# Kernel optimization log

Measured on AMD Instinct MI355X. Metric: run time of the kernel, lower is better.

The kernel has to match this reference:

```python
import jax, jax.numpy as jnp
import numpy as np

N = 100000
E = 1600000
F_IN = 128
HID = 32
HEADS = 4
NCLS = 64
NEG_SLOPE = 0.2
EPS = 1e-16


def setup_inputs() -> dict:
    key = jax.random.key(0)
    ks = jax.random.split(key, 12)
    inp = jax.random.normal(ks[0], (N, F_IN), dtype=jnp.float32)
    edge_index = jax.random.randint(ks[1], (2, E), 0, N, dtype=jnp.int64)
    s1 = 1.0 / np.sqrt(F_IN)
    W1 = jax.random.uniform(ks[2], (F_IN, HEADS, HID), jnp.float32, -s1, s1)
    att_src1 = jax.random.normal(ks[3], (HEADS, HID), dtype=jnp.float32) * s1
    att_dst1 = jax.random.normal(ks[4], (HEADS, HID), dtype=jnp.float32) * s1
    bias1 = jnp.zeros((HEADS * HID,), dtype=jnp.float32)
    d2 = HEADS * HID
    s2 = 1.0 / np.sqrt(d2)
    W2 = jax.random.uniform(ks[5], (d2, 1, NCLS), jnp.float32, -s2, s2)
    att_src2 = jax.random.normal(ks[6], (1, NCLS), dtype=jnp.float32) * s2
    att_dst2 = jax.random.normal(ks[7], (1, NCLS), dtype=jnp.float32) * s2
    bias2 = jnp.zeros((NCLS,), dtype=jnp.float32)
    return {"inp": inp, "edge_index": edge_index, "W1": W1, "att_src1": att_src1,
            "att_dst1": att_dst1, "bias1": bias1, "W2": W2, "att_src2": att_src2,
            "att_dst2": att_dst2, "bias2": bias2}


def _gat_layer(x, src, dst, W, a_src, a_dst, bias):
    # x: [N, F]; W: [F, H, C]
    h = jnp.einsum('nf,fhc->nhc', x, W)            # [N, H, C]
    a_s = jnp.sum(h * a_src[None], axis=-1)        # [N, H]
    a_d = jnp.sum(h * a_dst[None], axis=-1)        # [N, H]
    e = a_s[src] + a_d[dst]                        # [Etot, H]
    e = jnp.where(e >= 0, e, NEG_SLOPE * e)        # LeakyReLU(0.2)
    # softmax normalized per destination node (segment softmax)
    m = jax.ops.segment_max(e, dst, num_segments=N)      # [N, H]
    ex = jnp.exp(e - m[dst])
    denom = jax.ops.segment_sum(ex, dst, num_segments=N)  # [N, H]
    alpha = ex / (denom[dst] + EPS)                # [Etot, H]
    msg = h[src] * alpha[..., None]                # [Etot, H, C]
    out = jax.ops.segment_sum(msg, dst, num_segments=N)   # [N, H, C]
    return out.reshape(N, -1) + bias


def reference(inp, edge_index, W1, att_src1, att_dst1, bias1, W2, att_src2, att_dst2, bias2):
    # add self-loops (PyG GATConv default)
    loop = jnp.arange(N, dtype=edge_index.dtype)
    src = jnp.concatenate([edge_index[0], loop])
    dst = jnp.concatenate([edge_index[1], loop])
    x = _gat_layer(inp, src, dst, W1, att_src1, att_dst1, bias1)   # [N, H*HID]
    x = _gat_layer(x, src, dst, W2, att_src2, att_dst2, bias2)     # [N, NCLS]
    return x
```

## Files before the change

kernel.cpp:

```cpp
#include <hip/hip_runtime.h>

#define N_NODES 100000
#define F1 128
#define NCLS 64
#define EPB 8

typedef __attribute__((ext_vector_type(8))) short bf16x8;
typedef __attribute__((ext_vector_type(4))) float f32x4;

__device__ __forceinline__ unsigned f2bf(float x) {
    unsigned u = __builtin_bit_cast(unsigned, x);
    u += 0x7fff + ((u >> 16) & 1);
    return u >> 16;
}
__device__ __forceinline__ float bflo(unsigned u) {
    return __builtin_bit_cast(float, u << 16);
}
__device__ __forceinline__ float bfhi(unsigned u) {
    return __builtin_bit_cast(float, u & 0xffff0000u);
}

#define SWZ_I(v, off) __builtin_amdgcn_ds_swizzle((v), (off))
#define SWZ_F(v, off) __builtin_bit_cast(float, __builtin_amdgcn_ds_swizzle(__builtin_bit_cast(int, (v)), (off)))

__device__ __forceinline__ int load_edge(const int* ei, int is64, long long idx) {
    return is64 ? ei[2 * idx] : ei[idx];
}

#define EDGE_PROBE(ei, s_is64, tid) { \
    int v_ = (ei)[2 * ((tid) & 63) + 1]; \
    unsigned long long b_ = __ballot(v_ == 0); \
    if ((tid) == 0) s_is64 = (b_ == ~0ull) ? 1 : 0; }

__global__ __launch_bounds__(256) void histA_kernel(
        const int* __restrict__ ei, int* __restrict__ ghBM, int EB, int E) {
    __shared__ int bins[256];
    __shared__ int s_is64;
    int tid = threadIdx.x;
    bins[tid] = 0;
    EDGE_PROBE(ei, s_is64, tid)
    __syncthreads();
    int is64 = s_is64;
    long long base = (long long)blockIdx.x * 2048 + tid * EPB;
    int d[EPB];
    #pragma unroll
    for (int k = 0; k < EPB; ++k) {
        long long e = base + k;
        d[k] = (e < E) ? load_edge(ei, is64, (long long)E + e) : -1;
    }
    #pragma unroll
    for (int k = 0; k < EPB; ++k)
        if (d[k] >= 0) atomicAdd(&bins[d[k] >> 9], 1);
    __syncthreads();
    ghBM[(size_t)tid * EB + blockIdx.x] = bins[tid];
}

#define SCAN_BLOCK 1024
__global__ void pscanA_kernel(int* __restrict__ g, int* __restrict__ bsum, int K) {
    __shared__ int sm[SCAN_BLOCK];
    int tid = threadIdx.x;
    int i = blockIdx.x * SCAN_BLOCK + tid;
    int v = (i < K) ? g[i] : 0;
    sm[tid] = v;
    __syncthreads();
    for (int off = 1; off < SCAN_BLOCK; off <<= 1) {
        int t = (tid >= off) ? sm[tid - off] : 0;
        __syncthreads();
        sm[tid] += t;
        __syncthreads();
    }
    if (i < K) g[i] = sm[tid] - v;
    if (tid == SCAN_BLOCK - 1) bsum[blockIdx.x] = sm[tid];
}

__global__ void pscanC_kernel(int* __restrict__ g, const int* __restrict__ bsum,
                              int K, int nb) {
    __shared__ int sm[256];
    int tid = threadIdx.x;
    if (tid < 256) sm[tid] = (tid < nb) ? bsum[tid] : 0;
    __syncthreads();
    for (int off = 1; off < 256; off <<= 1) {
        int t = (tid < 256 && tid >= off) ? sm[tid - off] : 0;
        __syncthreads();
        if (tid < 256) sm[tid] += t;
        __syncthreads();
    }
    int pre = (blockIdx.x == 0) ? 0 : sm[blockIdx.x - 1];
    int i = blockIdx.x * SCAN_BLOCK + tid;
    if (i < K) g[i] += pre;
}

__global__ __launch_bounds__(256) void scatgemm1_kernel(
        const int* __restrict__ ei, const int* __restrict__ ghBM, int EB,
        unsigned* __restrict__ tmp, int E,
        const float* __restrict__ x, const float* __restrict__ W,
        const float* __restrict__ att_s, const float* __restrict__ att_d,
        unsigned* __restrict__ hp, float* __restrict__ as_, float* __restrict__ ad_, int n) {
    __shared__ uint4 WtS[2048];
    __shared__ int s_is64;
    int tid = threadIdx.x;
    if (blockIdx.x < (unsigned)EB) {
        int* base = (int*)WtS;
        base[tid] = ghBM[(size_t)tid * EB + blockIdx.x];
        EDGE_PROBE(ei, s_is64, tid)
        __syncthreads();
        int is64 = s_is64;
        long long eb = (long long)blockIdx.x * 2048 + tid * EPB;
        int d[EPB], s[EPB];
        #pragma unroll
        for (int k = 0; k < EPB; ++k) {
            long long e = eb + k;
            d[k] = (e < E) ? load_edge(ei, is64, (long long)E + e) : -1;
        }
        #pragma unroll
        for (int k = 0; k < EPB; ++k) {
            long long e = eb + k;
            s[k] = (e < E) ? load_edge(ei, is64, e) : 0;
        }
        #pragma unroll
        for (int k = 0; k < EPB; ++k) {
            if (d[k] >= 0) {
                int pos = atomicAdd(&base[d[k] >> 9], 1);
                tmp[pos] = (unsigned)s[k] | ((unsigned)(d[k] & 511) << 17);
            }
        }
        return;
    }
    unsigned* Wt = (unsigned*)WtS;
    {
        int ch = tid & 127, fb = tid >> 7;
        #pragma unroll
        for (int j8 = 0; j8 < 8; ++j8) {
            int f0 = fb * 64 + j8 * 8;
            unsigned pk[4];
            #pragma unroll
            for (int p = 0; p < 4; ++p) {
                float lo = W[(size_t)(f0 + 2 * p) * 128 + ch];
                float hi = W[(size_t)(f0 + 2 * p + 1) * 128 + ch];
                pk[p] = f2bf(lo) | (f2bf(hi) << 16);
            }
            int bcol = (f0 * 2) ^ ((ch & 7) << 4);
            *(uint4*)&Wt[ch * 64 + (bcol >> 2)] = *(uint4*)pk;
        }
    }
    __syncthreads();
    int lane = tid & 63, w = tid >> 6;
    int col = lane & 15, quad = lane >> 4;
    int nodebase = (blockIdx.x - EB) * 128 + w * 32;
    bf16x8 a[2][4];
    #pragma unroll
    for (int s = 0; s < 2; ++s) {
        int node = nodebase + s * 16 + col;
        const float* xr = x + (size_t)node * 128;
        bool v = node < n;
        #pragma unroll
        for (int kk = 0; kk < 4; ++kk) {
            float4 lo = v ? *(const float4*)&xr[kk * 32 + quad * 8]
                          : make_float4(0.f, 0.f, 0.f, 0.f);
            float4 hi = v ? *(const float4*)&xr[kk * 32 + quad * 8 + 4]
                          : make_float4(0.f, 0.f, 0.f, 0.f);
            unsigned pk[4];
            pk[0] = f2bf(lo.x) | (f2bf(lo.y) << 16);
            pk[1] = f2bf(lo.z) | (f2bf(lo.w) << 16);
            pk[2] = f2bf(hi.x) | (f2bf(hi.y) << 16);
            pk[3] = f2bf(hi.z) | (f2bf(hi.w) << 16);
            a[s][kk] = *(bf16x8*)pk;
        }
    }
    f32x4 acc[2][8] = {};
    #pragma unroll
    for (int c = 0; c < 8; ++c) {
        int brow = c * 16 + col;
        bf16x8 b[4];
        #pragma unroll
        for (int kk = 0; kk < 4; ++kk) {
            int bcol = (kk * 64 + quad * 16) ^ ((brow & 7) << 4);
            b[kk] = *(bf16x8*)&Wt[brow * 64 + (bcol >> 2)];
        }
        #pragma unroll
        for (int s = 0; s < 2; ++s)
            #pragma unroll
            for (int kk = 0; kk < 4; ++kk)
                acc[s][c] = __builtin_amdgcn_mfma_f32_16x16x32_bf16(a[s][kk], b[kk], acc[s][c], 0, 0, 0);
    }
    float aS[8], aD[8];
    #pragma unroll
    for (int c = 0; c < 8; ++c) { aS[c] = att_s[c * 16 + col]; aD[c] = att_d[c * 16 + col]; }
    #pragma unroll
    for (int s = 0; s < 2; ++s) {
        #pragma unroll
        for (int c = 0; c < 8; ++c) {
            #pragma unroll
            for (int r = 0; r < 4; ++r) {
                float own = acc[s][c][r];
                float par = SWZ_F(own, 0x041F);
                int node = nodebase + s * 16 + quad * 4 + r;
                if (!(lane & 1) && node < n)
                    hp[(size_t)node * 64 + c * 8 + (col >> 1)] =
                        f2bf(own) | (f2bf(par) << 16);
            }
        }
        #pragma unroll
        for (int h = 0; h < 4; ++h) {
            #pragma unroll
            for (int r = 0; r < 4; ++r) {
                float ps = acc[s][2 * h][r] * aS[2 * h] + acc[s][2 * h + 1][r] * aS[2 * h + 1];
                float pd = acc[s][2 * h][r] * aD[2 * h] + acc[s][2 * h + 1][r] * aD[2 * h + 1];
                ps += SWZ_F(ps, 0x041F); pd += SWZ_F(pd, 0x041F);
                ps += SWZ_F(ps, 0x081F); pd += SWZ_F(pd, 0x081F);
                ps += SWZ_F(ps, 0x101F); pd += SWZ_F(pd, 0x101F);
                ps += SWZ_F(ps, 0x201F); pd += SWZ_F(pd, 0x201F);
                int node = nodebase + s * 16 + quad * 4 + r;
                if (col == 0 && node < n) {
                    as_[(size_t)node * 4 + h] = ps;
                    ad_[(size_t)node * 4 + h] = pd;
                }
            }
        }
    }
}

__global__ __launch_bounds__(256) void bucketC_kernel(
        const unsigned* __restrict__ tmp, const int* __restrict__ ghBM, int EB,
        int* __restrict__ row_ptr, int* __restrict__ col, int E, int n) {
    __shared__ int lb[512];
    __shared__ int lo[512];
    __shared__ int sm[256];
    int bk = blockIdx.x;
    int tid = threadIdx.x;
    int gbase = ghBM[(size_t)bk * EB];
    int gend = (bk == 255) ? E : ghBM[(size_t)(bk + 1) * EB];
    int cnt = gend - gbase;
    lb[tid] = 0; lb[tid + 256] = 0;
    __syncthreads();
    for (int i = tid; i < cnt; i += 256)
        atomicAdd(&lb[tmp[gbase + i] >> 17], 1);
    __syncthreads();
    int p = lb[2 * tid], q = lb[2 * tid + 1];
    int ps = p + q;
    sm[tid] = ps;
    __syncthreads();
    for (int off = 1; off < 256; off <<= 1) {
        int t = (tid >= off) ? sm[tid - off] : 0;
        __syncthreads();
        sm[tid] += t;
        __syncthreads();
    }
    int excl = sm[tid] - ps;
    int e0 = excl, e1 = excl + p;
    lo[2 * tid] = e0; lo[2 * tid + 1] = e1;
    int v0 = bk * 512 + 2 * tid;
    if (v0 <= n) row_ptr[v0] = gbase + e0;
    if (v0 + 1 <= n) row_ptr[v0 + 1] = gbase + e1;
    __syncthreads();
    for (int i = tid; i < cnt; i += 256) {
        unsigned v = tmp[gbase + i];
        int r = atomicAdd(&lo[v >> 17], 1);
        col[gbase + r] = (int)(v & 0x1FFFFu);
    }
}

__global__ __launch_bounds__(256) void gemm2_kernel(
        const unsigned* __restrict__ xp, const float* __restrict__ W,
        const float* __restrict__ att_s, const float* __restrict__ att_d,
        unsigned* __restrict__ hp, float* __restrict__ as_, float* __restrict__ ad_, int n) {
    __shared__ uint4 WtS[1024];
    unsigned* Wt = (unsigned*)WtS;
    int tid = threadIdx.x;
    {
        int ch = tid & 63, fb = tid >> 6;
        #pragma unroll
        for (int j8 = 0; j8 < 4; ++j8) {
            int f0 = fb * 32 + j8 * 8;
            unsigned pk[4];
            #pragma unroll
            for (int p = 0; p < 4; ++p) {
                float lo = W[(size_t)(f0 + 2 * p) * 64 + ch];
                float hi = W[(size_t)(f0 + 2 * p + 1) * 64 + ch];
                pk[p] = f2bf(lo) | (f2bf(hi) << 16);
            }
            int bcol = (f0 * 2) ^ ((ch & 7) << 4);
            *(uint4*)&Wt[ch * 64 + (bcol >> 2)] = *(uint4*)pk;
        }
    }
    __syncthreads();
    int lane = tid & 63, w = tid >> 6;
    int col = lane & 15, quad = lane >> 4;
    int nodebase = blockIdx.x * 128 + w * 32;
    bf16x8 a[2][4];
    #pragma unroll
    for (int s = 0; s < 2; ++s) {
        int node = nodebase + s * 16 + col;
        bool v = node < n;
        #pragma unroll
        for (int kk = 0; kk < 4; ++kk) {
            uint4 u = v ? *(const uint4*)&xp[(size_t)node * 64 + kk * 16 + quad * 4]
                        : make_uint4(0, 0, 0, 0);
            a[s][kk] = *(bf16x8*)&u;
        }
    }
    f32x4 acc[2][4] = {};
    #pragma unroll
    for (int c = 0; c < 4; ++c) {
        int brow = c * 16 + col;
        bf16x8 b[4];
        #pragma unroll
        for (int kk = 0; kk < 4; ++kk) {
            int bcol = (kk * 64 + quad * 16) ^ ((brow & 7) << 4);
            b[kk] = *(bf16x8*)&Wt[brow * 64 + (bcol >> 2)];
        }
        #pragma unroll
        for (int s = 0; s < 2; ++s)
            #pragma unroll
            for (int kk = 0; kk < 4; ++kk)
                acc[s][c] = __builtin_amdgcn_mfma_f32_16x16x32_bf16(a[s][kk], b[kk], acc[s][c], 0, 0, 0);
    }
    float aS[4], aD[4];
    #pragma unroll
    for (int c = 0; c < 4; ++c) { aS[c] = att_s[c * 16 + col]; aD[c] = att_d[c * 16 + col]; }
    #pragma unroll
    for (int s = 0; s < 2; ++s) {
        #pragma unroll
        for (int c = 0; c < 4; ++c) {
            #pragma unroll
            for (int r = 0; r < 4; ++r) {
                float own = acc[s][c][r];
                float par = SWZ_F(own, 0x041F);
                int node = nodebase + s * 16 + quad * 4 + r;
                if (!(lane & 1) && node < n)
                    hp[(size_t)node * 32 + c * 8 + (col >> 1)] =
                        f2bf(own) | (f2bf(par) << 16);
            }
        }
        #pragma unroll
        for (int r = 0; r < 4; ++r) {
            float ps = 0.f, pd = 0.f;
            #pragma unroll
            for (int c = 0; c < 4; ++c) {
                ps = fmaf(acc[s][c][r], aS[c], ps);
                pd = fmaf(acc[s][c][r], aD[c], pd);
            }
            ps += SWZ_F(ps, 0x041F); pd += SWZ_F(pd, 0x041F);
            ps += SWZ_F(ps, 0x081F); pd += SWZ_F(pd, 0x081F);
            ps += SWZ_F(ps, 0x101F); pd += SWZ_F(pd, 0x101F);
            ps += SWZ_F(ps, 0x201F); pd += SWZ_F(pd, 0x201F);
            int node = nodebase + s * 16 + quad * 4 + r;
            if (col == 0 && node < n) { as_[node] = ps; ad_[node] = pd; }
        }
    }
}

#define A1_G8(B, K0) { \
    int t0 = SWZ_I(myc, (((B)+(K0)+0)<<5)); \
    int t1 = SWZ_I(myc, (((B)+(K0)+1)<<5)); \
    int t2 = SWZ_I(myc, (((B)+(K0)+2)<<5)); \
    int t3 = SWZ_I(myc, (((B)+(K0)+3)<<5)); \
    int t4 = SWZ_I(myc, (((B)+(K0)+4)<<5)); \
    int t5 = SWZ_I(myc, (((B)+(K0)+5)<<5)); \
    int t6 = SWZ_I(myc, (((B)+(K0)+6)<<5)); \
    int t7 = SWZ_I(myc, (((B)+(K0)+7)<<5)); \
    unsigned v0 = hp[(size_t)t0 * 64 + lane]; \
    unsigned v1 = hp[(size_t)t1 * 64 + lane]; \
    unsigned v2 = hp[(size_t)t2 * 64 + lane]; \
    unsigned v3 = hp[(size_t)t3 * 64 + lane]; \
    unsigned v4 = hp[(size_t)t4 * 64 + lane]; \
    unsigned v5 = hp[(size_t)t5 * 64 + lane]; \
    unsigned v6 = hp[(size_t)t6 * 64 + lane]; \
    unsigned v7 = hp[(size_t)t7 * 64 + lane]; \
    float q0 = SWZ_F(ew, ((((K0)+0)<<5)|0x10)); \
    float q1 = SWZ_F(ew, ((((K0)+1)<<5)|0x10)); \
    float q2 = SWZ_F(ew, ((((K0)+2)<<5)|0x10)); \
    float q3 = SWZ_F(ew, ((((K0)+3)<<5)|0x10)); \
    float q4 = SWZ_F(ew, ((((K0)+4)<<5)|0x10)); \
    float q5 = SWZ_F(ew, ((((K0)+5)<<5)|0x10)); \
    float q6 = SWZ_F(ew, ((((K0)+6)<<5)|0x10)); \
    float q7 = SWZ_F(ew, ((((K0)+7)<<5)|0x10)); \
    s += q0; acc0 = fmaf(q0, bflo(v0), acc0); acc1 = fmaf(q0, bfhi(v0), acc1); \
    s += q1; acc0 = fmaf(q1, bflo(v1), acc0); acc1 = fmaf(q1, bfhi(v1), acc1); \
    s += q2; acc0 = fmaf(q2, bflo(v2), acc0); acc1 = fmaf(q2, bfhi(v2), acc1); \
    s += q3; acc0 = fmaf(q3, bflo(v3), acc0); acc1 = fmaf(q3, bfhi(v3), acc1); \
    s += q4; acc0 = fmaf(q4, bflo(v4), acc0); acc1 = fmaf(q4, bfhi(v4), acc1); \
    s += q5; acc0 = fmaf(q5, bflo(v5), acc0); acc1 = fmaf(q5, bfhi(v5), acc1); \
    s += q6; acc0 = fmaf(q6, bflo(v6), acc0); acc1 = fmaf(q6, bfhi(v6), acc1); \
    s += q7; acc0 = fmaf(q7, bflo(v7), acc0); acc1 = fmaf(q7, bfhi(v7), acc1); }

#define A1_SUB(B) { \
    int sspec = SWZ_I(myc, (((B)<<5) | 0x0F)); \
    float ee_ = as_[(size_t)sspec * 4 + head] + adv; \
    ee_ = fmaxf(ee_, 0.2f * ee_); \
    float ew = ((cb + (B) + (lane & 15)) < end) ? __expf(ee_) : 0.f; \
    A1_G8(B, 0) \
    if (m > (B) + 8) A1_G8(B, 8) }

__global__ __launch_bounds__(256) void agg1_kernel(
        const unsigned* __restrict__ hp, const float* __restrict__ as_,
        const float* __restrict__ ad_, const int* __restrict__ row_ptr,
        const int* __restrict__ col, const float* __restrict__ bias,
        unsigned* __restrict__ outp, int n) {
    int wid = (blockIdx.x * 256 + threadIdx.x) >> 6;
    int lane = threadIdx.x & 63;
    if (wid >= n) return;
    int node = wid;
    int head = lane >> 4;
    float adv = ad_[(size_t)node * 4 + head];
    float e0 = as_[(size_t)node * 4 + head] + adv;
    e0 = fmaxf(e0, 0.2f * e0);
    float w0 = __expf(e0);
    float s = w0;
    unsigned u0 = hp[(size_t)node * 64 + lane];
    float acc0 = w0 * bflo(u0), acc1 = w0 * bfhi(u0);
    int beg = row_ptr[node], end = row_ptr[node + 1];
    for (int cb = beg; cb < end; cb += 32) {
        int m = end - cb; if (m > 32) m = 32;
        int ci = cb + (lane & 31);
        int myc = col[(ci < end) ? ci : (end - 1)];
        A1_SUB(0)
        if (m > 16) A1_SUB(16)
    }
    float inv = 1.0f / (s + 1e-16f);
    float2 b = *(const float2*)&bias[lane * 2];
    outp[(size_t)node * 64 + lane] =
        f2bf(acc0 * inv + b.x) | (f2bf(acc1 * inv + b.y) << 16);
}

#define A2_G4(K0) { \
    int t0 = SWZ_I(myc, (((K0)+0)<<5)); \
    int t1 = SWZ_I(myc, (((K0)+1)<<5)); \
    int t2 = SWZ_I(myc, (((K0)+2)<<5)); \
    int t3 = SWZ_I(myc, (((K0)+3)<<5)); \
    unsigned v0 = hp[(size_t)t0 * 32 + wrd]; \
    unsigned v1 = hp[(size_t)t1 * 32 + wrd]; \
    unsigned v2 = hp[(size_t)t2 * 32 + wrd]; \
    unsigned v3 = hp[(size_t)t3 * 32 + wrd]; \
    float q0 = SWZ_F(ew, (((K0)+0)<<5)); \
    float q1 = SWZ_F(ew, (((K0)+1)<<5)); \
    float q2 = SWZ_F(ew, (((K0)+2)<<5)); \
    float q3 = SWZ_F(ew, (((K0)+3)<<5)); \
    s += q0; acc0 = fmaf(q0, bflo(v0), acc0); acc1 = fmaf(q0, bfhi(v0), acc1); \
    s += q1; acc0 = fmaf(q1, bflo(v1), acc0); acc1 = fmaf(q1, bfhi(v1), acc1); \
    s += q2; acc0 = fmaf(q2, bflo(v2), acc0); acc1 = fmaf(q2, bfhi(v2), acc1); \
    s += q3; acc0 = fmaf(q3, bflo(v3), acc0); acc1 = fmaf(q3, bfhi(v3), acc1); }

__global__ __launch_bounds__(256) void agg2_kernel(
        const unsigned* __restrict__ hp, const float* __restrict__ as_,
        const float* __restrict__ ad_, const int* __restrict__ row_ptr,
        const int* __restrict__ col, const float* __restrict__ bias,
        float* __restrict__ out, int n) {
    int wid = (blockIdx.x * 256 + threadIdx.x) >> 6;
    int lane = threadIdx.x & 63;
    if (wid >= n) return;
    int node = wid;
    int half = lane >> 5, wrd = lane & 31;
    float adv = ad_[node];
    float s = 0.f, acc0 = 0.f, acc1 = 0.f;
    {
        float e = as_[node] + adv; e = fmaxf(e, 0.2f * e);
        float w = __expf(e);
        if (half == 0) {
            unsigned u = hp[(size_t)node * 32 + wrd];
            s = w; acc0 = w * bflo(u); acc1 = w * bfhi(u);
        }
    }
    int beg = row_ptr[node], end = row_ptr[node + 1];
    for (int cb = beg; cb < end; cb += 64) {
        int m = end - cb; if (m > 64) m = 64;
        int idx = cb + 2 * (lane & 31) + half;
        int myc = col[(idx < end) ? idx : (end - 1)];
        float ee = as_[myc] + adv; ee = fmaxf(ee, 0.2f * ee);
        float ew = (idx < end) ? __expf(ee) : 0.f;
        A2_G4(0)
        if (m > 8)  A2_G4(4)
        if (m > 16) A2_G4(8)
        if (m > 24) A2_G4(12)
        if (m > 32) {
            A2_G4(16)
            if (m > 40) A2_G4(20)
            if (m > 48) A2_G4(24)
            if (m > 56) A2_G4(28)
        }
    }
    s += __shfl_xor(s, 32);
    acc0 += __shfl_xor(acc0, 32);
    acc1 += __shfl_xor(acc1, 32);
    if (half == 0) {
        float inv = 1.0f / (s + 1e-16f);
        float2 b = *(const float2*)&bias[wrd * 2];
        *(float2*)&out[(size_t)node * 64 + wrd * 2] =
            make_float2(acc0 * inv + b.x, acc1 * inv + b.y);
    }
}

extern "C" void kernel_launch(void* const* d_in, const int* in_sizes, int n_in,
                              void* d_out, int out_size, void* d_ws, size_t ws_size,
                              hipStream_t stream) {
    const float* inp   = (const float*)d_in[0];
    const int*   ei    = (const int*)d_in[1];
    const float* W1    = (const float*)d_in[2];
    const float* atts1 = (const float*)d_in[3];
    const float* attd1 = (const float*)d_in[4];
    const float* bias1 = (const float*)d_in[5];
    const float* W2    = (const float*)d_in[6];
    const float* atts2 = (const float*)d_in[7];
    const float* attd2 = (const float*)d_in[8];
    const float* bias2 = (const float*)d_in[9];
    float* out = (float*)d_out;

    const int N = N_NODES;
    const int E = in_sizes[1] / 2;

    const int EB = (E + 2047) / 2048;
    const int K = 256 * EB;
    const int nbK = (K + SCAN_BLOCK - 1) / SCAN_BLOCK;
    const int nG1 = (N + 127) / 128;

    unsigned* h1p = (unsigned*)d_ws;
    unsigned* x1p = h1p + (size_t)N * 64;
    float* as1 = (float*)(x1p + (size_t)N * 64);
    float* ad1 = as1 + (size_t)N * 4;
    int* row_ptr  = (int*)(ad1 + (size_t)N * 4);
    int* col      = row_ptr + N + 1;
    int* ghBM     = col + E;
    int* bsum     = ghBM + K;
    unsigned* tmp = x1p;

    histA_kernel<<<EB, 256, 0, stream>>>(ei, ghBM, EB, E);
    pscanA_kernel<<<nbK, SCAN_BLOCK, 0, stream>>>(ghBM, bsum, K);
    pscanC_kernel<<<nbK, SCAN_BLOCK, 0, stream>>>(ghBM, bsum, K, nbK);
    scatgemm1_kernel<<<EB + nG1, 256, 0, stream>>>(
        ei, ghBM, EB, tmp, E, inp, W1, atts1, attd1, h1p, as1, ad1, N);
    bucketC_kernel<<<256, 256, 0, stream>>>(tmp, ghBM, EB, row_ptr, col, E, N);

    agg1_kernel<<<(N + 3) / 4, 256, 0, stream>>>(h1p, as1, ad1, row_ptr, col, bias1, x1p, N);

    gemm2_kernel<<<(N + 127) / 128, 256, 0, stream>>>(x1p, W2, atts2, attd2, h1p, as1, ad1, N);
    agg2_kernel<<<(N + 3) / 4, 256, 0, stream>>>(h1p, as1, ad1, row_ptr, col, bias2, out, N);
}
```

Baseline: 210.2 us.

## Fuse histogram with GEMM1, fold block-sum scan into scatter, stage buckets in LDS

The edge histogram now runs inside the GEMM1 launch instead of as a separate kernel, and the scatter step becomes its own kernel. The second scan pass (pscanC) is removed; the scatter and bucket kernels each rescan the block sums in shared memory to rebuild global offsets. The bucket kernel caches its segment of tmp in a 48KB LDS buffer so the count pass and the placement pass both read it from there instead of global memory. This trades one fewer launch and fewer global reads for redundant per-block scans and higher LDS use, which may lower occupancy in the bucket kernel.

New measurement: 204.7 us (median of 2 runs). 1.03x faster.

```diff
diff --git a/kernel.cpp b/kernel.cpp
--- a/kernel.cpp
+++ b/kernel.cpp
@@ -4,6 +4,7 @@
 #define F1 128
 #define NCLS 64
 #define EPB 8
+#define BCAP 12288
 
 typedef __attribute__((ext_vector_type(8))) short bf16x8;
 typedef __attribute__((ext_vector_type(4))) float f32x4;
@@ -32,67 +33,18 @@
     unsigned long long b_ = __ballot(v_ == 0); \
     if ((tid) == 0) s_is64 = (b_ == ~0ull) ? 1 : 0; }
 
-__global__ __launch_bounds__(256) void histA_kernel(
-        const int* __restrict__ ei, int* __restrict__ ghBM, int EB, int E) {
-    __shared__ int bins[256];
-    __shared__ int s_is64;
-    int tid = threadIdx.x;
-    bins[tid] = 0;
-    EDGE_PROBE(ei, s_is64, tid)
-    __syncthreads();
-    int is64 = s_is64;
-    long long base = (long long)blockIdx.x * 2048 + tid * EPB;
-    int d[EPB];
-    #pragma unroll
-    for (int k = 0; k < EPB; ++k) {
-        long long e = base + k;
-        d[k] = (e < E) ? load_edge(ei, is64, (long long)E + e) : -1;
-    }
-    #pragma unroll
-    for (int k = 0; k < EPB; ++k)
-        if (d[k] >= 0) atomicAdd(&bins[d[k] >> 9], 1);
-    __syncthreads();
-    ghBM[(size_t)tid * EB + blockIdx.x] = bins[tid];
-}
-
-#define SCAN_BLOCK 1024
-__global__ void pscanA_kernel(int* __restrict__ g, int* __restrict__ bsum, int K) {
-    __shared__ int sm[SCAN_BLOCK];
-    int tid = threadIdx.x;
-    int i = blockIdx.x * SCAN_BLOCK + tid;
-    int v = (i < K) ? g[i] : 0;
-    sm[tid] = v;
-    __syncthreads();
-    for (int off = 1; off < SCAN_BLOCK; off <<= 1) {
-        int t = (tid >= off) ? sm[tid - off] : 0;
-        __syncthreads();
-        sm[tid] += t;
-        __syncthreads();
-    }
-    if (i < K) g[i] = sm[tid] - v;
-    if (tid == SCAN_BLOCK - 1) bsum[blockIdx.x] = sm[tid];
-}
-
-__global__ void pscanC_kernel(int* __restrict__ g, const int* __restrict__ bsum,
-                              int K, int nb) {
-    __shared__ int sm[256];
-    int tid = threadIdx.x;
-    if (tid < 256) sm[tid] = (tid < nb) ? bsum[tid] : 0;
-    __syncthreads();
-    for (int off = 1; off < 256; off <<= 1) {
-        int t = (tid < 256 && tid >= off) ? sm[tid - off] : 0;
-        __syncthreads();
-        if (tid < 256) sm[tid] += t;
-        __syncthreads();
-    }
-    int pre = (blockIdx.x == 0) ? 0 : sm[blockIdx.x - 1];
-    int i = blockIdx.x * SCAN_BLOCK + tid;
-    if (i < K) g[i] += pre;
-}
-
-__global__ __launch_bounds__(256) void scatgemm1_kernel(
-        const int* __restrict__ ei, const int* __restrict__ ghBM, int EB,
-        unsigned* __restrict__ tmp, int E,
+#define BSUM_SCAN(sm, bsum, nb, tid) { \
+    sm[tid] = ((tid) < (nb)) ? bsum[tid] : 0; \
+    __syncthreads(); \
+    for (int off_ = 1; off_ < 256; off_ <<= 1) { \
+        int t_ = ((tid) >= off_) ? sm[(tid) - off_] : 0; \
+        __syncthreads(); \
+        sm[tid] += t_; \
+        __syncthreads(); \
+    } }
+
+__global__ __launch_bounds__(256) void histgemm1_kernel(
+        const int* __restrict__ ei, int* __restrict__ ghBM, int EB, int E,
         const float* __restrict__ x, const float* __restrict__ W,
         const float* __restrict__ att_s, const float* __restrict__ att_d,
         unsigned* __restrict__ hp, float* __restrict__ as_, float* __restrict__ ad_, int n) {
@@ -100,30 +52,23 @@
     __shared__ int s_is64;
     int tid = threadIdx.x;
     if (blockIdx.x < (unsigned)EB) {
-        int* base = (int*)WtS;
-        base[tid] = ghBM[(size_t)tid * EB + blockIdx.x];
+        int* bins = (int*)WtS;
+        bins[tid] = 0;
         EDGE_PROBE(ei, s_is64, tid)
         __syncthreads();
         int is64 = s_is64;
-        long long eb = (long long)blockIdx.x * 2048 + tid * EPB;
-        int d[EPB], s[EPB];
+        long long base = (long long)blockIdx.x * 2048 + tid * EPB;
+        int d[EPB];
         #pragma unroll
         for (int k = 0; k < EPB; ++k) {
-            long long e = eb + k;
+            long long e = base + k;
             d[k] = (e < E) ? load_edge(ei, is64, (long long)E + e) : -1;
         }
         #pragma unroll
-        for (int k = 0; k < EPB; ++k) {
-            long long e = eb + k;
-            s[k] = (e < E) ? load_edge(ei, is64, e) : 0;
-        }
-        #pragma unroll
-        for (int k = 0; k < EPB; ++k) {
-            if (d[k] >= 0) {
-                int pos = atomicAdd(&base[d[k] >> 9], 1);
-                tmp[pos] = (unsigned)s[k] | ((unsigned)(d[k] & 511) << 17);
-            }
-        }
+        for (int k = 0; k < EPB; ++k)
+            if (d[k] >= 0) atomicAdd(&bins[d[k] >> 9], 1);
+        __syncthreads();
+        ghBM[(size_t)tid * EB + blockIdx.x] = bins[tid];
         return;
     }
     unsigned* Wt = (unsigned*)WtS;
@@ -220,21 +165,98 @@
     }
 }
 
+#define SCAN_BLOCK 1024
+__global__ void pscanA_kernel(int* __restrict__ g, int* __restrict__ bsum, int K) {
+    __shared__ int sm[SCAN_BLOCK];
+    int tid = threadIdx.x;
+    int i = blockIdx.x * SCAN_BLOCK + tid;
+    int v = (i < K) ? g[i] : 0;
+    sm[tid] = v;
+    __syncthreads();
+    for (int off = 1; off < SCAN_BLOCK; off <<= 1) {
+        int t = (tid >= off) ? sm[tid - off] : 0;
+        __syncthreads();
+        sm[tid] += t;
+        __syncthreads();
+    }
+    if (i < K) g[i] = sm[tid] - v;
+    if (tid == SCAN_BLOCK - 1) bsum[blockIdx.x] = sm[tid];
+}
+
+__global__ __launch_bounds__(256) void scatterB_kernel(
+        const int* __restrict__ ei, const int* __restrict__ ghBM, int EB,
+        const int* __restrict__ bsum, int nbK,
+        unsigned* __restrict__ tmp, int E) {
+    __shared__ int base[256];
+    __shared__ int sm[256];
+    __shared__ int s_is64;
+    int tid = threadIdx.x;
+    EDGE_PROBE(ei, s_is64, tid)
+    BSUM_SCAN(sm, bsum, nbK, tid)
+    {
+        int idx = tid * EB + blockIdx.x;
+        int chunk = idx >> 10;
+        int pre = (chunk == 0) ? 0 : sm[chunk - 1];
+        base[tid] = ghBM[(size_t)idx] + pre;
+    }
+    __syncthreads();
+    int is64 = s_is64;
+    long long eb = (long long)blockIdx.x * 2048 + tid * EPB;
+    int d[EPB], s[EPB];
+    #pragma unroll
+    for (int k = 0; k < EPB; ++k) {
+        long long e = eb + k;
+        d[k] = (e < E) ? load_edge(ei, is64, (long long)E + e) : -1;
+    }
+    #pragma unroll
+    for (int k = 0; k < EPB; ++k) {
+        long long e = eb + k;
+        s[k] = (e < E) ? load_edge(ei, is64, e) : 0;
+    }
+    #pragma unroll
+    for (int k = 0; k < EPB; ++k) {
+        if (d[k] >= 0) {
+            int pos = atomicAdd(&base[d[k] >> 9], 1);
+            tmp[pos] = (unsigned)s[k] | ((unsigned)(d[k] & 511) << 17);
+        }
+    }
+}
+
 __global__ __launch_bounds__(256) void bucketC_kernel(
         const unsigned* __restrict__ tmp, const int* __restrict__ ghBM, int EB,
+        const int* __restrict__ bsum, int nbK,
         int* __restrict__ row_ptr, int* __restrict__ col, int E, int n) {
+    __shared__ unsigned stmp[BCAP];
     __shared__ int lb[512];
     __shared__ int lo[512];
     __shared__ int sm[256];
     int bk = blockIdx.x;
     int tid = threadIdx.x;
-    int gbase = ghBM[(size_t)bk * EB];
-    int gend = (bk == 255) ? E : ghBM[(size_t)(bk + 1) * EB];
+    BSUM_SCAN(sm, bsum, nbK, tid)
+    int i0 = bk * EB;
+    int c0 = (i0 >> 10), p0 = (c0 == 0) ? 0 : sm[c0 - 1];
+    int gbase = ghBM[(size_t)i0] + p0;
+    int gend = E;
+    if (bk < 255) {
+        int i1 = (bk + 1) * EB;
+        int c1 = (i1 >> 10), p1 = (c1 == 0) ? 0 : sm[c1 - 1];
+        gend = ghBM[(size_t)i1] + p1;
+    }
     int cnt = gend - gbase;
+    bool lds = (cnt <= BCAP);
+    __syncthreads();
     lb[tid] = 0; lb[tid + 256] = 0;
-    __syncthreads();
-    for (int i = tid; i < cnt; i += 256)
-        atomicAdd(&lb[tmp[gbase + i] >> 17], 1);
+    if (lds) {
+        for (int i = tid; i < cnt; i += 256) stmp[i] = tmp[gbase + i];
+    }
+    __syncthreads();
+    if (lds) {
+        for (int i = tid; i < cnt; i += 256)
+            atomicAdd(&lb[stmp[i] >> 17], 1);
+    } else {
+        for (int i = tid; i < cnt; i += 256)
+            atomicAdd(&lb[tmp[gbase + i] >> 17], 1);
+    }
     __syncthreads();
     int p = lb[2 * tid], q = lb[2 * tid + 1];
     int ps = p + q;
@@ -253,10 +275,18 @@
     if (v0 <= n) row_ptr[v0] = gbase + e0;
     if (v0 + 1 <= n) row_ptr[v0 + 1] = gbase + e1;
     __syncthreads();
-    for (int i = tid; i < cnt; i += 256) {
-        unsigned v = tmp[gbase + i];
-        int r = atomicAdd(&lo[v >> 17], 1);
-        col[gbase + r] = (int)(v & 0x1FFFFu);
+    if (lds) {
+        for (int i = tid; i < cnt; i += 256) {
+            unsigned v = stmp[i];
+            int r = atomicAdd(&lo[v >> 17], 1);
+            col[gbase + r] = (int)(v & 0x1FFFFu);
+        }
+    } else {
+        for (int i = tid; i < cnt; i += 256) {
+            unsigned v = tmp[gbase + i];
+            int r = atomicAdd(&lo[v >> 17], 1);
+            col[gbase + r] = (int)(v & 0x1FFFFu);
+        }
     }
 }
 
@@ -523,12 +553,11 @@
     int* bsum     = ghBM + K;
     unsigned* tmp = x1p;
 
-    histA_kernel<<<EB, 256, 0, stream>>>(ei, ghBM, EB, E);
+    histgemm1_kernel<<<EB + nG1, 256, 0, stream>>>(
+        ei, ghBM, EB, E, inp, W1, atts1, attd1, h1p, as1, ad1, N);
     pscanA_kernel<<<nbK, SCAN_BLOCK, 0, stream>>>(ghBM, bsum, K);
-    pscanC_kernel<<<nbK, SCAN_BLOCK, 0, stream>>>(ghBM, bsum, K, nbK);
-    scatgemm1_kernel<<<EB + nG1, 256, 0, stream>>>(
-        ei, ghBM, EB, tmp, E, inp, W1, atts1, attd1, h1p, as1, ad1, N);
-    bucketC_kernel<<<256, 256, 0, stream>>>(tmp, ghBM, EB, row_ptr, col, E, N);
+    scatterB_kernel<<<EB, 256, 0, stream>>>(ei, ghBM, EB, bsum, nbK, tmp, E);
+    bucketC_kernel<<<256, 256, 0, stream>>>(tmp, ghBM, EB, bsum, nbK, row_ptr, col, E, N);
 
     agg1_kernel<<<(N + 3) / 4, 256, 0, stream>>>(h1p, as1, ad1, row_ptr, col, bias1, x1p, N);
 
```
